# Optimization experiments

Measured on AMD Instinct MI355X. Metric: run time of the kernel, lower is better.

## Reference

```python
import jax, jax.numpy as jnp
import numpy as np

B, S, H = 2, 2048, 1024
NH, HD = 16, 64  # num heads, head dim
EPS = 1e-12


def setup_inputs() -> dict:
    key = jax.random.key(0)
    ks = jax.random.split(key, 10)
    sc = 1.0 / np.sqrt(H)
    return {
        "hidden_states": jax.random.normal(ks[0], (B, S, H), jnp.float32),
        "Wq": jax.random.normal(ks[1], (H, H), jnp.float32) * sc,
        "bq": jnp.zeros((H,), jnp.float32),
        "Wk": jax.random.normal(ks[2], (H, H), jnp.float32) * sc,
        "bk": jnp.zeros((H,), jnp.float32),
        "Wv": jax.random.normal(ks[3], (H, H), jnp.float32) * sc,
        "bv": jnp.zeros((H,), jnp.float32),
        "Wo": jax.random.normal(ks[4], (H, H), jnp.float32) * sc,
        "bo": jnp.zeros((H,), jnp.float32),
        "ln_g": jnp.ones((H,), jnp.float32),
        "ln_b": jnp.zeros((H,), jnp.float32),
    }


def reference(hidden_states, Wq, bq, Wk, bk, Wv, bv, Wo, bo, ln_g, ln_b):
    x = hidden_states  # [B,S,H]
    def split_heads(t):
        return t.reshape(B, S, NH, HD).transpose(0, 2, 1, 3)  # [B,NH,S,HD]
    q = split_heads(x @ Wq.T + bq)
    k = split_heads(x @ Wk.T + bk)
    v = split_heads(x @ Wv.T + bv)
    scores = jnp.einsum("bhqd,bhkd->bhqk", q, k) / np.sqrt(HD)
    causal = jnp.tril(jnp.ones((S, S), bool))  # [S,S]
    scores = jnp.where(causal[None, None], scores, -jnp.inf)
    probs = jax.nn.softmax(scores, axis=-1)
    ctx = jnp.einsum("bhqk,bhkd->bhqd", probs, v)
    ctx = ctx.transpose(0, 2, 1, 3).reshape(B, S, H)
    attn_out = ctx @ Wo.T + bo
    y = attn_out + x
    mu = jnp.mean(y, axis=-1, keepdims=True)
    var = jnp.mean((y - mu) ** 2, axis=-1, keepdims=True)
    return (y - mu) / jnp.sqrt(var + EPS) * ln_g + ln_b
```

## Files before the change

### kernel.cpp

```cpp
#include <hip/hip_runtime.h>

#define B_  2
#define S_  2048
#define H_  1024
#define NH_ 16
#define HD_ 64
#define M_  (B_*S_)

typedef __attribute__((ext_vector_type(8))) __bf16 bf16x8;
typedef __attribute__((ext_vector_type(4))) float  f32x4;
typedef __attribute__((ext_vector_type(8))) unsigned short us8;
typedef __attribute__((ext_vector_type(4))) float  fl4;

__device__ __forceinline__ unsigned short f2bf(float f) {
    unsigned int u = __float_as_uint(f);
    u += 0x7fffu + ((u >> 16) & 1u);
    return (unsigned short)(u >> 16);
}

__global__ __launch_bounds__(256) void cast_kernel(
    const float* __restrict__ x,
    const float* __restrict__ wq, const float* __restrict__ wk,
    const float* __restrict__ wv, const float* __restrict__ wo,
    unsigned short* __restrict__ xb, unsigned short* __restrict__ wb) {
    size_t t  = (size_t)blockIdx.x * 256 + threadIdx.x;
    size_t e0 = t * 4;
    const size_t XN = (size_t)M_ * H_;
    const float* src;
    unsigned short* dst;
    if (e0 < XN) { src = x + e0; dst = xb + e0; }
    else {
        size_t j = e0 - XN;
        int w = (int)(j >> 20);
        size_t off = j & ((1u << 20) - 1);
        const float* wp = (w == 0) ? wq : (w == 1) ? wk : (w == 2) ? wv : wo;
        src = wp + off; dst = wb + j;
    }
    fl4 v = *(const fl4*)src;
    ushort4 o;
    o.x = f2bf(v.x); o.y = f2bf(v.y); o.z = f2bf(v.z); o.w = f2bf(v.w);
    *(ushort4*)dst = o;
}

__global__ __launch_bounds__(512) void gemm_qkv(
    const unsigned short* __restrict__ xb, const unsigned short* __restrict__ wb,
    const float* __restrict__ bq, const float* __restrict__ bk,
    const float* __restrict__ bv,
    unsigned short* __restrict__ qb, unsigned short* __restrict__ kbuf,
    unsigned short* __restrict__ vT) {
    __shared__ __align__(16) unsigned short As[128 * 72];
    __shared__ __align__(16) unsigned short Bs[128 * 72];
    const int z = blockIdx.z;
    const unsigned short* W = wb + ((size_t)z << 20);
    const int m0 = blockIdx.x * 128, n0 = blockIdx.y * 128;
    const int t = threadIdx.x, lane = t & 63, w = t >> 6;
    const int wm = w >> 2, wn = w & 3;
    const int quad = lane >> 4, l16 = lane & 15;
    const int sr = t >> 2, sc = (t & 3) * 16;
    const unsigned short* ga = xb + (size_t)(m0 + sr) * H_ + sc;
    const unsigned short* gb = W  + (size_t)(n0 + sr) * H_ + sc;

    us8 a0 = *(const us8*)(ga),     a1 = *(const us8*)(ga + 8);
    us8 b0 = *(const us8*)(gb),     b1 = *(const us8*)(gb + 8);

    f32x4 acc[4][2] = {};
    for (int k0 = 0; k0 < H_; k0 += 64) {
        if (k0) __syncthreads();
        *(us8*)&As[sr * 72 + sc]     = a0;  *(us8*)&As[sr * 72 + sc + 8] = a1;
        *(us8*)&Bs[sr * 72 + sc]     = b0;  *(us8*)&Bs[sr * 72 + sc + 8] = b1;
        __syncthreads();
        if (k0 + 64 < H_) {
            ga += 64; gb += 64;
            a0 = *(const us8*)(ga);  a1 = *(const us8*)(ga + 8);
            b0 = *(const us8*)(gb);  b1 = *(const us8*)(gb + 8);
        }
#pragma unroll
        for (int kk = 0; kk < 64; kk += 32) {
            bf16x8 af[4], bfr[2];
#pragma unroll
            for (int i = 0; i < 4; i++)
                af[i]  = *(const bf16x8*)&As[(wm * 64 + i * 16 + l16) * 72 + kk + quad * 8];
#pragma unroll
            for (int jn = 0; jn < 2; jn++)
                bfr[jn] = *(const bf16x8*)&Bs[(wn * 32 + jn * 16 + l16) * 72 + kk + quad * 8];
#pragma unroll
            for (int mi = 0; mi < 4; mi++)
#pragma unroll
                for (int ni = 0; ni < 2; ni++)
                    acc[mi][ni] = __builtin_amdgcn_mfma_f32_16x16x32_bf16(
                        af[mi], bfr[ni], acc[mi][ni], 0, 0, 0);
        }
    }
    const float* bias = (z == 0) ? bq : (z == 1) ? bk : bv;
    if (z == 2) {
#pragma unroll
        for (int mi = 0; mi < 4; mi++) {
#pragma unroll
            for (int ni = 0; ni < 2; ni++) {
                int col  = n0 + wn * 32 + ni * 16 + l16;
                float bval = bias[col];
                int row0 = m0 + wm * 64 + mi * 16 + quad * 4;
                int bb = row0 >> 11, s0 = row0 & 2047;
                ushort4 pk;
                pk.x = f2bf(acc[mi][ni][0] + bval);
                pk.y = f2bf(acc[mi][ni][1] + bval);
                pk.z = f2bf(acc[mi][ni][2] + bval);
                pk.w = f2bf(acc[mi][ni][3] + bval);
                *(ushort4*)&vT[((size_t)bb * NH_ * HD_ + col) * S_ + s0] = pk;
            }
        }
    } else {
        unsigned short* out = (z == 0) ? qb : kbuf;
        const float qs = (z == 0) ? 0.18033688f : 1.0f;
#pragma unroll
        for (int mi = 0; mi < 4; mi++) {
#pragma unroll
            for (int ni = 0; ni < 2; ni++) {
                int col = n0 + wn * 32 + ni * 16 + l16;
                float bval = bias[col];
#pragma unroll
                for (int r = 0; r < 4; r++) {
                    int row = m0 + wm * 64 + mi * 16 + quad * 4 + r;
                    out[(size_t)row * H_ + col] = f2bf((acc[mi][ni][r] + bval) * qs);
                }
            }
        }
    }
}

__global__ __launch_bounds__(512) void gemm_out(
    const unsigned short* __restrict__ ctxb, const unsigned short* __restrict__ wob,
    const float* __restrict__ bo, const float* __restrict__ x,
    float* __restrict__ y) {
    __shared__ __align__(16) unsigned short As[128 * 72];
    __shared__ __align__(16) unsigned short Bs[128 * 72];
    const int m0 = blockIdx.x * 128, n0 = blockIdx.y * 128;
    const int t = threadIdx.x, lane = t & 63, w = t >> 6;
    const int wm = w >> 2, wn = w & 3;
    const int quad = lane >> 4, l16 = lane & 15;
    const int sr = t >> 2, sc = (t & 3) * 16;
    const unsigned short* ga = ctxb + (size_t)(m0 + sr) * H_ + sc;
    const unsigned short* gb = wob  + (size_t)(n0 + sr) * H_ + sc;

    us8 a0 = *(const us8*)(ga),     a1 = *(const us8*)(ga + 8);
    us8 b0 = *(const us8*)(gb),     b1 = *(const us8*)(gb + 8);

    f32x4 acc[4][2] = {};
    for (int k0 = 0; k0 < H_; k0 += 64) {
        if (k0) __syncthreads();
        *(us8*)&As[sr * 72 + sc]     = a0;  *(us8*)&As[sr * 72 + sc + 8] = a1;
        *(us8*)&Bs[sr * 72 + sc]     = b0;  *(us8*)&Bs[sr * 72 + sc + 8] = b1;
        __syncthreads();
        if (k0 + 64 < H_) {
            ga += 64; gb += 64;
            a0 = *(const us8*)(ga);  a1 = *(const us8*)(ga + 8);
            b0 = *(const us8*)(gb);  b1 = *(const us8*)(gb + 8);
        }
#pragma unroll
        for (int kk = 0; kk < 64; kk += 32) {
            bf16x8 af[4], bfr[2];
#pragma unroll
            for (int i = 0; i < 4; i++)
                af[i]  = *(const bf16x8*)&As[(wm * 64 + i * 16 + l16) * 72 + kk + quad * 8];
#pragma unroll
            for (int jn = 0; jn < 2; jn++)
                bfr[jn] = *(const bf16x8*)&Bs[(wn * 32 + jn * 16 + l16) * 72 + kk + quad * 8];
#pragma unroll
            for (int mi = 0; mi < 4; mi++)
#pragma unroll
                for (int ni = 0; ni < 2; ni++)
                    acc[mi][ni] = __builtin_amdgcn_mfma_f32_16x16x32_bf16(
                        af[mi], bfr[ni], acc[mi][ni], 0, 0, 0);
        }
    }
#pragma unroll
    for (int mi = 0; mi < 4; mi++) {
#pragma unroll
        for (int ni = 0; ni < 2; ni++) {
            int col = n0 + wn * 32 + ni * 16 + l16;
            float bval = bo[col];
#pragma unroll
            for (int r = 0; r < 4; r++) {
                size_t idx = (size_t)(m0 + wm * 64 + mi * 16 + quad * 4 + r) * H_ + col;
                y[idx] = acc[mi][ni][r] + bval + x[idx];
            }
        }
    }
}

__global__ __launch_bounds__(512, 4) void attn_kernel(
    const unsigned short* __restrict__ qb, const unsigned short* __restrict__ kb,
    const unsigned short* __restrict__ vT, unsigned short* __restrict__ ctxb) {
    __shared__ __align__(16) unsigned short Ks[2][128 * 68];
    __shared__ __align__(16) unsigned short Vt[2][64 * 132];
    __shared__ __align__(16) unsigned short Ps[128 * 44];
    const int flat = blockIdx.x;
    const int rnd  = flat >> 8;
    const int within = flat & 255;
    const int xcd = within & 7, s2 = within >> 3;
    const int bh  = xcd * 4 + (s2 >> 3);
    const int j   = s2 & 7;
    const int fj  = (j & 1) ? (15 - j) : j;
    const int p2  = rnd ? (15 - fj) : fj;
    const int b = bh >> 4, h = bh & 15;
    const int t = threadIdx.x, lane = t & 63, wid = t >> 6;
    const int quad = lane >> 4, l16 = lane & 15;
    const int skr = t >> 2, skc = (t & 3) * 16;
    const int svr = t >> 3, svc = (t & 7) * 16;
    const size_t headoff = (size_t)h * HD_;
    const unsigned short* vtb = vT + ((size_t)(b * NH_ + h) * HD_) * S_;
    const int qrow = wid * 16 + l16;

    const int q0 = p2 * 128;
    const int nsteps = p2 + 1;

    const size_t qr = (size_t)(b * S_ + q0 + qrow);
    bf16x8 qva = *(const bf16x8*)(qb + qr * H_ + headoff + quad * 8);
    bf16x8 qvb = *(const bf16x8*)(qb + qr * H_ + headoff + 32 + quad * 8);

    float m1 = -1e30f, l1 = 0.f;
    f32x4 o1[4] = {};

    const unsigned short* kptr = kb  + (size_t)(b * S_ + skr) * H_ + headoff + skc;
    const unsigned short* vptr = vtb + (size_t)svr * S_ + svc;
    us8 nk0 = *(const us8*)kptr,  nk1 = *(const us8*)(kptr + 8);
    us8 nv0 = *(const us8*)vptr,  nv1 = *(const us8*)(vptr + 8);
    *(us8*)&Ks[0][skr * 68 + skc]      = nk0;
    *(us8*)&Ks[0][skr * 68 + skc + 8]  = nk1;
    *(us8*)&Vt[0][svr * 132 + svc]     = nv0;
    *(us8*)&Vt[0][svr * 132 + svc + 8] = nv1;
    __syncthreads();

    for (int s = 0; s < nsteps; s++) {
        const int buf = s & 1;
        const bool pf = (s + 1 < nsteps);
        if (pf) {
            kptr += (size_t)128 * H_;
            vptr += 128;
            nk0 = *(const us8*)kptr;  nk1 = *(const us8*)(kptr + 8);
            nv0 = *(const us8*)vptr;  nv1 = *(const us8*)(vptr + 8);
        }
        f32x4 sacc[8] = {};
        __builtin_amdgcn_s_setprio(1);
#pragma unroll
        for (int kk = 0; kk < 64; kk += 32) {
            bf16x8 bqf = (kk == 0) ? qva : qvb;
#pragma unroll
            for (int nt = 0; nt < 8; nt++) {
                bf16x8 ak = *(const bf16x8*)&Ks[buf][(nt * 16 + l16) * 68 + kk + quad * 8];
                sacc[nt] = __builtin_amdgcn_mfma_f32_16x16x32_bf16(ak, bqf, sacc[nt], 0, 0, 0);
            }
        }
        __builtin_amdgcn_s_setprio(0);
        if (s == p2) {
#pragma unroll
            for (int nt = 0; nt < 8; nt++) {
#pragma unroll
                for (int r = 0; r < 4; r++) {
                    int key = nt * 16 + quad * 4 + r;
                    if (key > qrow) sacc[nt][r] = -1e30f;
                }
            }
        }
        float tm[8];
#pragma unroll
        for (int nt = 0; nt < 8; nt++)
            tm[nt] = fmaxf(fmaxf(sacc[nt][0], sacc[nt][1]), fmaxf(sacc[nt][2], sacc[nt][3]));
        float mx = fmaxf(fmaxf(fmaxf(tm[0], tm[1]), fmaxf(tm[2], tm[3])),
                         fmaxf(fmaxf(tm[4], tm[5]), fmaxf(tm[6], tm[7])));
        mx = fmaxf(mx, __shfl_xor(mx, 16));
        mx = fmaxf(mx, __shfl_xor(mx, 32));
        const bool skip = __all(mx <= m1 + 5.0f);
        float m_new = skip ? m1 : fmaxf(m1, mx);
        float ss = 0.f;
        ushort4 pks[8];
#pragma unroll
        for (int nt = 0; nt < 8; nt++) {
            float p0 = __builtin_amdgcn_exp2f(sacc[nt][0] - m_new);
            float p1 = __builtin_amdgcn_exp2f(sacc[nt][1] - m_new);
            float p2e = __builtin_amdgcn_exp2f(sacc[nt][2] - m_new);
            float p3 = __builtin_amdgcn_exp2f(sacc[nt][3] - m_new);
            ss += (p0 + p1) + (p2e + p3);
            pks[nt].x = (unsigned short)(__float_as_uint(p0) >> 16);
            pks[nt].y = (unsigned short)(__float_as_uint(p1) >> 16);
            pks[nt].z = (unsigned short)(__float_as_uint(p2e) >> 16);
            pks[nt].w = (unsigned short)(__float_as_uint(p3) >> 16);
        }
        ss += __shfl_xor(ss, 16);
        ss += __shfl_xor(ss, 32);
        if (skip) {
            l1 += ss;
        } else {
            float alpha = __builtin_amdgcn_exp2f(m1 - m_new);
            l1 = l1 * alpha + ss;
            m1 = m_new;
#pragma unroll
            for (int dt = 0; dt < 4; dt++)
#pragma unroll
                for (int r = 0; r < 4; r++) o1[dt][r] *= alpha;
        }
        __builtin_amdgcn_s_setprio(1);
#pragma unroll
        for (int kk = 0; kk < 128; kk += 32) {
            const int nb = kk >> 4;
            *(ushort4*)&Ps[(wid * 16 + l16) * 44 + quad * 4]      = pks[nb];
            *(ushort4*)&Ps[(wid * 16 + l16) * 44 + 16 + quad * 4] = pks[nb + 1];
            bf16x8 pfr = *(const bf16x8*)&Ps[(wid * 16 + l16) * 44 + quad * 8];
#pragma unroll
            for (int dt = 0; dt < 4; dt++) {
                bf16x8 vf = *(const bf16x8*)&Vt[buf][(dt * 16 + l16) * 132 + kk + quad * 8];
                o1[dt] = __builtin_amdgcn_mfma_f32_16x16x32_bf16(vf, pfr, o1[dt], 0, 0, 0);
            }
        }
        __builtin_amdgcn_s_setprio(0);
        if (pf) {
            *(us8*)&Ks[buf ^ 1][skr * 68 + skc]      = nk0;
            *(us8*)&Ks[buf ^ 1][skr * 68 + skc + 8]  = nk1;
            *(us8*)&Vt[buf ^ 1][svr * 132 + svc]     = nv0;
            *(us8*)&Vt[buf ^ 1][svr * 132 + svc + 8] = nv1;
            __syncthreads();
        }
    }
    {
        const float inv = 1.0f / l1;
        size_t row = (size_t)(b * S_ + q0 + qrow);
#pragma unroll
        for (int dt = 0; dt < 4; dt++) {
            ushort4 pk;
            pk.x = f2bf(o1[dt][0] * inv);
            pk.y = f2bf(o1[dt][1] * inv);
            pk.z = f2bf(o1[dt][2] * inv);
            pk.w = f2bf(o1[dt][3] * inv);
            *(ushort4*)&ctxb[row * H_ + headoff + dt * 16 + quad * 4] = pk;
        }
    }
}

__global__ __launch_bounds__(256) void ln_kernel(
    const float* __restrict__ y, const float* __restrict__ g,
    const float* __restrict__ bta, float* __restrict__ out) {
    __shared__ float red[8];
    const int row = blockIdx.x, t = threadIdx.x;
    fl4 v = *(const fl4*)(y + (size_t)row * H_ + t * 4);
    float s  = v.x + v.y + v.z + v.w;
    float sq = v.x * v.x + v.y * v.y + v.z * v.z + v.w * v.w;
    for (int m = 1; m < 64; m <<= 1) { s += __shfl_xor(s, m); sq += __shfl_xor(sq, m); }
    const int wid = t >> 6, lane = t & 63;
    if (lane == 0) { red[wid * 2] = s; red[wid * 2 + 1] = sq; }
    __syncthreads();
    s  = red[0] + red[2] + red[4] + red[6];
    sq = red[1] + red[3] + red[5] + red[7];
    float mu   = s * (1.0f / H_);
    float var  = sq * (1.0f / H_) - mu * mu;
    float rstd = rsqrtf(fmaxf(var, 0.f) + 1e-12f);
    fl4 gg = *(const fl4*)(g + t * 4);
    fl4 bb = *(const fl4*)(bta + t * 4);
    fl4 o;
    o.x = (v.x - mu) * rstd * gg.x + bb.x;
    o.y = (v.y - mu) * rstd * gg.y + bb.y;
    o.z = (v.z - mu) * rstd * gg.z + bb.z;
    o.w = (v.w - mu) * rstd * gg.w + bb.w;
    *(fl4*)(out + (size_t)row * H_ + t * 4) = o;
}

extern "C" void kernel_launch(void* const* d_in, const int* in_sizes, int n_in,
                              void* d_out, int out_size, void* d_ws, size_t ws_size,
                              hipStream_t stream) {
    const float* x  = (const float*)d_in[0];
    const float* Wq = (const float*)d_in[1];
    const float* bq = (const float*)d_in[2];
    const float* Wk = (const float*)d_in[3];
    const float* bk = (const float*)d_in[4];
    const float* Wv = (const float*)d_in[5];
    const float* bv = (const float*)d_in[6];
    const float* Wo = (const float*)d_in[7];
    const float* bo = (const float*)d_in[8];
    const float* lg = (const float*)d_in[9];
    const float* lb = (const float*)d_in[10];
    float* out = (float*)d_out;

    const size_t MEG = 1024u * 1024u;
    unsigned short* ws16 = (unsigned short*)d_ws;
    unsigned short* xb   = ws16;
    unsigned short* wb   = ws16 + 4 * MEG;
    unsigned short* qb   = ws16 + 8 * MEG;
    unsigned short* kb   = ws16 + 12 * MEG;
    unsigned short* vT   = ws16 + 16 * MEG;
    unsigned short* ctxb = ws16 + 20 * MEG;
    float* y = (float*)(ws16 + 24 * MEG);

    cast_kernel<<<8192, 256, 0, stream>>>(x, Wq, Wk, Wv, Wo, xb, wb);
    gemm_qkv<<<dim3(32, 8, 3), 512, 0, stream>>>(xb, wb, bq, bk, bv, qb, kb, vT);
    attn_kernel<<<dim3(512), 512, 0, stream>>>(qb, kb, vT, ctxb);
    gemm_out<<<dim3(32, 8), 512, 0, stream>>>(ctxb, wb + 3 * MEG, bo, x, y);
    ln_kernel<<<4096, 256, 0, stream>>>(y, lg, lb, out);
}
```

Baseline: 190.4 us.

## Stage GEMM tiles with direct global-to-LDS loads instead of register staging

```diff
diff --git a/kernel.cpp b/kernel.cpp
--- a/kernel.cpp
+++ b/kernel.cpp
@@ -48,41 +48,42 @@
     const float* __restrict__ bv,
     unsigned short* __restrict__ qb, unsigned short* __restrict__ kbuf,
     unsigned short* __restrict__ vT) {
-    __shared__ __align__(16) unsigned short As[128 * 72];
-    __shared__ __align__(16) unsigned short Bs[128 * 72];
+    __shared__ __align__(16) unsigned short As[128 * 64];
+    __shared__ __align__(16) unsigned short Bs[128 * 64];
     const int z = blockIdx.z;
     const unsigned short* W = wb + ((size_t)z << 20);
     const int m0 = blockIdx.x * 128, n0 = blockIdx.y * 128;
     const int t = threadIdx.x, lane = t & 63, w = t >> 6;
     const int wm = w >> 2, wn = w & 3;
     const int quad = lane >> 4, l16 = lane & 15;
-    const int sr = t >> 2, sc = (t & 3) * 16;
-    const unsigned short* ga = xb + (size_t)(m0 + sr) * H_ + sc;
-    const unsigned short* gb = W  + (size_t)(n0 + sr) * H_ + sc;
-
-    us8 a0 = *(const us8*)(ga),     a1 = *(const us8*)(ga + 8);
-    us8 b0 = *(const us8*)(gb),     b1 = *(const us8*)(gb + 8);
+    const int srow = w * 8 + (lane >> 3);
+    const int scol = (lane & 7) * 8;
+    const unsigned short* gA0 = xb + (size_t)(m0 + srow) * H_ + scol;
+    const unsigned short* gA1 = xb + (size_t)(m0 + 64 + srow) * H_ + scol;
+    const unsigned short* gB0 = W  + (size_t)(n0 + srow) * H_ + scol;
+    const unsigned short* gB1 = W  + (size_t)(n0 + 64 + srow) * H_ + scol;
+    unsigned short* lA0 = &As[(w * 8) * 64];
+    unsigned short* lA1 = &As[(64 + w * 8) * 64];
+    unsigned short* lB0 = &Bs[(w * 8) * 64];
+    unsigned short* lB1 = &Bs[(64 + w * 8) * 64];
 
     f32x4 acc[4][2] = {};
     for (int k0 = 0; k0 < H_; k0 += 64) {
         if (k0) __syncthreads();
-        *(us8*)&As[sr * 72 + sc]     = a0;  *(us8*)&As[sr * 72 + sc + 8] = a1;
-        *(us8*)&Bs[sr * 72 + sc]     = b0;  *(us8*)&Bs[sr * 72 + sc + 8] = b1;
+        __builtin_amdgcn_global_load_lds((const unsigned int*)(gA0 + k0), (unsigned int*)lA0, 16, 0, 0);
+        __builtin_amdgcn_global_load_lds((const unsigned int*)(gA1 + k0), (unsigned int*)lA1, 16, 0, 0);
+        __builtin_amdgcn_global_load_lds((const unsigned int*)(gB0 + k0), (unsigned int*)lB0, 16, 0, 0);
+        __builtin_amdgcn_global_load_lds((const unsigned int*)(gB1 + k0), (unsigned int*)lB1, 16, 0, 0);
         __syncthreads();
-        if (k0 + 64 < H_) {
-            ga += 64; gb += 64;
-            a0 = *(const us8*)(ga);  a1 = *(const us8*)(ga + 8);
-            b0 = *(const us8*)(gb);  b1 = *(const us8*)(gb + 8);
-        }
 #pragma unroll
         for (int kk = 0; kk < 64; kk += 32) {
             bf16x8 af[4], bfr[2];
 #pragma unroll
             for (int i = 0; i < 4; i++)
-                af[i]  = *(const bf16x8*)&As[(wm * 64 + i * 16 + l16) * 72 + kk + quad * 8];
+                af[i]  = *(const bf16x8*)&As[(wm * 64 + i * 16 + l16) * 64 + kk + quad * 8];
 #pragma unroll
             for (int jn = 0; jn < 2; jn++)
-                bfr[jn] = *(const bf16x8*)&Bs[(wn * 32 + jn * 16 + l16) * 72 + kk + quad * 8];
+                bfr[jn] = *(const bf16x8*)&Bs[(wn * 32 + jn * 16 + l16) * 64 + kk + quad * 8];
 #pragma unroll
             for (int mi = 0; mi < 4; mi++)
 #pragma unroll
@@ -132,39 +133,40 @@
     const unsigned short* __restrict__ ctxb, const unsigned short* __restrict__ wob,
     const float* __restrict__ bo, const float* __restrict__ x,
     float* __restrict__ y) {
-    __shared__ __align__(16) unsigned short As[128 * 72];
-    __shared__ __align__(16) unsigned short Bs[128 * 72];
+    __shared__ __align__(16) unsigned short As[128 * 64];
+    __shared__ __align__(16) unsigned short Bs[128 * 64];
     const int m0 = blockIdx.x * 128, n0 = blockIdx.y * 128;
     const int t = threadIdx.x, lane = t & 63, w = t >> 6;
     const int wm = w >> 2, wn = w & 3;
     const int quad = lane >> 4, l16 = lane & 15;
-    const int sr = t >> 2, sc = (t & 3) * 16;
-    const unsigned short* ga = ctxb + (size_t)(m0 + sr) * H_ + sc;
-    const unsigned short* gb = wob  + (size_t)(n0 + sr) * H_ + sc;
-
-    us8 a0 = *(const us8*)(ga),     a1 = *(const us8*)(ga + 8);
-    us8 b0 = *(const us8*)(gb),     b1 = *(const us8*)(gb + 8);
+    const int srow = w * 8 + (lane >> 3);
+    const int scol = (lane & 7) * 8;
+    const unsigned short* gA0 = ctxb + (size_t)(m0 + srow) * H_ + scol;
+    const unsigned short* gA1 = ctxb + (size_t)(m0 + 64 + srow) * H_ + scol;
+    const unsigned short* gB0 = wob  + (size_t)(n0 + srow) * H_ + scol;
+    const unsigned short* gB1 = wob  + (size_t)(n0 + 64 + srow) * H_ + scol;
+    unsigned short* lA0 = &As[(w * 8) * 64];
+    unsigned short* lA1 = &As[(64 + w * 8) * 64];
+    unsigned short* lB0 = &Bs[(w * 8) * 64];
+    unsigned short* lB1 = &Bs[(64 + w * 8) * 64];
 
     f32x4 acc[4][2] = {};
     for (int k0 = 0; k0 < H_; k0 += 64) {
         if (k0) __syncthreads();
-        *(us8*)&As[sr * 72 + sc]     = a0;  *(us8*)&As[sr * 72 + sc + 8] = a1;
-        *(us8*)&Bs[sr * 72 + sc]     = b0;  *(us8*)&Bs[sr * 72 + sc + 8] = b1;
+        __builtin_amdgcn_global_load_lds((const unsigned int*)(gA0 + k0), (unsigned int*)lA0, 16, 0, 0);
+        __builtin_amdgcn_global_load_lds((const unsigned int*)(gA1 + k0), (unsigned int*)lA1, 16, 0, 0);
+        __builtin_amdgcn_global_load_lds((const unsigned int*)(gB0 + k0), (unsigned int*)lB0, 16, 0, 0);
+        __builtin_amdgcn_global_load_lds((const unsigned int*)(gB1 + k0), (unsigned int*)lB1, 16, 0, 0);
         __syncthreads();
-        if (k0 + 64 < H_) {
-            ga += 64; gb += 64;
-            a0 = *(const us8*)(ga);  a1 = *(const us8*)(ga + 8);
-            b0 = *(const us8*)(gb);  b1 = *(const us8*)(gb + 8);
-        }
 #pragma unroll
         for (int kk = 0; kk < 64; kk += 32) {
             bf16x8 af[4], bfr[2];
 #pragma unroll
             for (int i = 0; i < 4; i++)
-                af[i]  = *(const bf16x8*)&As[(wm * 64 + i * 16 + l16) * 72 + kk + quad * 8];
+                af[i]  = *(const bf16x8*)&As[(wm * 64 + i * 16 + l16) * 64 + kk + quad * 8];
 #pragma unroll
             for (int jn = 0; jn < 2; jn++)
-                bfr[jn] = *(const bf16x8*)&Bs[(wn * 32 + jn * 16 + l16) * 72 + kk + quad * 8];
+                bfr[jn] = *(const bf16x8*)&Bs[(wn * 32 + jn * 16 + l16) * 64 + kk + quad * 8];
 #pragma unroll
             for (int mi = 0; mi < 4; mi++)
 #pragma unroll
```

New measurement: 215.1 us. 13.0% more time.
